# Optimization experiments

Measured on AMD Instinct MI355X. Metric: run time of the kernel, lower is better.

## Reference

```python
import jax, jax.numpy as jnp
import numpy as np

EPS = 1e-7
CP_NUM = 16
P_NUM_TOTAL = 1024
P_PER_SEG = P_NUM_TOTAL // CP_NUM  # 64, matches int(p_num / cp_num)
ALPHA = 0.5


def setup_inputs() -> dict:
    key = jax.random.key(0)
    cps = jax.random.normal(key, (16384, CP_NUM, 2), dtype=jnp.float32)
    return {"cps": cps}


def reference(cps):
    # Centripetal Catmull-Rom spline sampling (closed curve), fully vectorized
    # over segments and sample points instead of the original double Python loop.
    B, S, D = cps.shape  # S == cp_num
    P = P_PER_SEG

    # Close the curve: append first control point.  [B, S+1, D]
    cc = jnp.concatenate([cps, cps[:, :1, :]], axis=1)

    # Boundary extension lengths (detached in the original via .detach_()).
    l01 = jax.lax.stop_gradient(
        jnp.sqrt(jnp.sum((cc[:, 0] - cc[:, 1]) ** 2, axis=-1) + EPS))[:, None]
    llast = jax.lax.stop_gradient(
        jnp.sqrt(jnp.sum((cc[:, -1] - cc[:, -2]) ** 2, axis=-1) + EPS))[:, None]
    aux_first = cc[:, 0] - l01 / llast * (cc[:, -1] - cc[:, -2])
    aux_last = cc[:, -1] + llast / l01 * (cc[:, 1] - cc[:, 0])
    # Auxiliary control points. [B, S+3, D]
    aux = jnp.concatenate([aux_first[:, None], cc, aux_last[:, None]], axis=1)

    # Centripetal knot vector: t[i] = t[i-1] + ||aux_i - aux_{i-1}||^alpha (detached).
    seg_len = jnp.sqrt(jnp.sum((aux[:, 1:] - aux[:, :-1]) ** 2, axis=-1)) ** ALPHA
    t = jnp.concatenate(
        [jnp.zeros((B, 1), dtype=cps.dtype), jnp.cumsum(seg_len, axis=1)], axis=1)
    t = jax.lax.stop_gradient(t)  # [B, S+3]

    idx = jnp.arange(S)
    # Knot windows per segment, broadcast to [B, S, 1, 1].
    t0 = t[:, idx][:, :, None, None]
    t1 = t[:, idx + 1][:, :, None, None]
    t2 = t[:, idx + 2][:, :, None, None]
    t3 = t[:, idx + 3][:, :, None, None]
    # Control point windows per segment, broadcast to [B, S, 1, D].
    P0 = aux[:, idx][:, :, None, :]
    P1 = aux[:, idx + 1][:, :, None, :]
    P2 = aux[:, idx + 2][:, :, None, :]
    P3 = aux[:, idx + 3][:, :, None, :]

    # batch_linspace(t1, t2, P): P points inclusive of both endpoints. [B,S,P,1]
    u = jnp.linspace(0.0, 1.0, P, dtype=cps.dtype)[None, None, :, None]
    tv = t1 + (t2 - t1) * u

    # Barry-Goldman pyramid of weighted blends.
    x01 = (t1 - tv) / (t1 - t0) * P0 + (tv - t0) / (t1 - t0) * P1
    x12 = (t2 - tv) / (t2 - t1) * P1 + (tv - t1) / (t2 - t1) * P2
    x23 = (t3 - tv) / (t3 - t2) * P2 + (tv - t2) / (t3 - t2) * P3
    x012 = (t2 - tv) / (t2 - t0) * x01 + (tv - t0) / (t2 - t0) * x12
    x123 = (t3 - tv) / (t3 - t1) * x12 + (tv - t1) / (t3 - t1) * x23
    pts = (t2 - tv) / (t2 - t1) * x012 + (tv - t1) / (t2 - t1) * x123  # [B,S,P,D]

    return pts.reshape(B, S * P, D)
```

## Files before the change

### kernel.cpp

```cpp
#include <hip/hip_runtime.h>

#define CP_NUM 16
#define SEGS   16
#define WPB    4
#define BLK    (WPB * 64)

__global__ __launch_bounds__(BLK) void spline_poly_kernel(
    const float* __restrict__ cps, float* __restrict__ out, int nb)
{
    __shared__ __align__(16) float s_cp [WPB][CP_NUM * 2];
    __shared__ __align__(16) float s_aux[WPB][19 * 2];
    __shared__ __align__(16) float s_t  [WPB][20];
    __shared__ __align__(16) float s_seg[WPB][SEGS][12];

    const int lane = threadIdx.x & 63;
    const int wv   = threadIdx.x >> 6;
    const int b    = blockIdx.x * WPB + wv;
    if (b >= nb) return;

    if (lane < 8) {
        reinterpret_cast<float4*>(s_cp[wv])[lane] =
            reinterpret_cast<const float4*>(cps + (size_t)b * (CP_NUM * 2))[lane];
    }
    __builtin_amdgcn_wave_barrier();

    if (lane < 19) {
        const float c0x = s_cp[wv][0],  c0y = s_cp[wv][1];
        const float c1x = s_cp[wv][2],  c1y = s_cp[wv][3];
        const float cLx = s_cp[wv][30], cLy = s_cp[wv][31];
        const float dx01 = c0x - c1x, dy01 = c0y - c1y;
        const float l01   = sqrtf(dx01 * dx01 + dy01 * dy01 + 1e-7f);
        const float dxl = c0x - cLx, dyl = c0y - cLy;
        const float llast = sqrtf(dxl * dxl + dyl * dyl + 1e-7f);
        float ax, ay;
        if (lane == 0) {
            const float r = l01 / llast;
            ax = c0x - r * dxl;  ay = c0y - r * dyl;
        } else if (lane <= CP_NUM) {
            ax = s_cp[wv][(lane - 1) * 2];  ay = s_cp[wv][(lane - 1) * 2 + 1];
        } else if (lane == CP_NUM + 1) {
            ax = c0x;  ay = c0y;
        } else {
            const float r = llast / l01;
            ax = c0x + r * (c1x - c0x);  ay = c0y + r * (c1y - c0y);
        }
        s_aux[wv][lane * 2]     = ax;
        s_aux[wv][lane * 2 + 1] = ay;
    }
    __builtin_amdgcn_wave_barrier();

    float len = 0.f;
    if (lane < 18) {
        const float dx = s_aux[wv][(lane + 1) * 2]     - s_aux[wv][lane * 2];
        const float dy = s_aux[wv][(lane + 1) * 2 + 1] - s_aux[wv][lane * 2 + 1];
        len = sqrtf(sqrtf(dx * dx + dy * dy));
    }
    #pragma unroll
    for (int d = 1; d < 32; d <<= 1) {
        const float n = __shfl_up(len, d);
        if (lane >= d) len += n;
    }
    if (lane == 0) s_t[wv][0] = 0.f;
    if (lane < 18) s_t[wv][lane + 1] = len;
    __builtin_amdgcn_wave_barrier();

    if (lane < SEGS) {
        const float t0 = s_t[wv][lane];
        const float t1 = s_t[wv][lane + 1];
        const float t2 = s_t[wv][lane + 2];
        const float t3 = s_t[wv][lane + 3];
        const float A  = t1 - t0, Bk = t2 - t1, C = t3 - t2;
        const float BC = Bk + C;
        const float r10 = 1.f / A;
        const float r21 = 1.f / Bk;
        const float r32 = 1.f / C;
        const float r20 = 1.f / (A + Bk);
        const float r31 = 1.f / BC;

        float* sp = s_seg[wv][lane];
        #pragma unroll
        for (int d = 0; d < 2; ++d) {
            const float P0 = s_aux[wv][lane * 2 + d];
            const float P1 = s_aux[wv][lane * 2 + 2 + d];
            const float P2 = s_aux[wv][lane * 2 + 4 + d];
            const float P3 = s_aux[wv][lane * 2 + 6 + d];
            const float L1c0 = P1,                              L1c1 = (P1 - P0) * r10;
            const float L2c0 = P1,                              L2c1 = (P2 - P1) * r21;
            const float L3c0 = (BC * P2 - Bk * P3) * r32,       L3c1 = (P3 - P2) * r32;
            const float Q1c0 = r20 * (Bk * L1c0 + A * L2c0);
            const float Q1c1 = r20 * (Bk * L1c1 - L1c0 + A * L2c1 + L2c0);
            const float Q1c2 = r20 * (L2c1 - L1c1);
            const float Q2c0 = r31 * (BC * L2c0);
            const float Q2c1 = r31 * (BC * L2c1 - L2c0 + L3c0);
            const float Q2c2 = r31 * (L3c1 - L2c1);
            sp[d * 4 + 0] = Q1c0;
            sp[d * 4 + 1] = Q1c1 + r21 * (Q2c0 - Q1c0);
            sp[d * 4 + 2] = Q1c2 + r21 * (Q2c1 - Q1c1);
            sp[d * 4 + 3] = r21 * (Q2c2 - Q1c2);
        }
        sp[8] = Bk;
    }
    __builtin_amdgcn_wave_barrier();

    float4* outw = reinterpret_cast<float4*>(out + (size_t)b * (SEGS * 64 * 2));
    #pragma unroll
    for (int i = 0; i < 8; ++i) {
        const int f  = lane + 64 * i;
        const int sg = f >> 5;
        const int j  = (f & 31) * 2;
        const float* sp = s_seg[wv][sg];
        const float4 cx = *reinterpret_cast<const float4*>(sp);
        const float4 cy = *reinterpret_cast<const float4*>(sp + 4);
        const float dt  = sp[8];
        const float s0 = dt * (float)j       * (1.f / 63.f);
        const float s1 = dt * (float)(j + 1) * (1.f / 63.f);
        float4 o;
        o.x = ((cx.w * s0 + cx.z) * s0 + cx.y) * s0 + cx.x;
        o.y = ((cy.w * s0 + cy.z) * s0 + cy.y) * s0 + cy.x;
        o.z = ((cx.w * s1 + cx.z) * s1 + cx.y) * s1 + cx.x;
        o.w = ((cy.w * s1 + cy.z) * s1 + cy.y) * s1 + cy.x;
        outw[f] = o;
    }
}

extern "C" void kernel_launch(void* const* d_in, const int* in_sizes, int n_in,
                              void* d_out, int out_size, void* d_ws, size_t ws_size,
                              hipStream_t stream) {
    const float* cps = (const float*)d_in[0];
    float* out = (float*)d_out;
    const int B = in_sizes[0] / (CP_NUM * 2);
    const int grid = (B + WPB - 1) / WPB;
    spline_poly_kernel<<<grid, BLK, 0, stream>>>(cps, out, B);
}
```

Before: 27.74 us.

## Replace LDS staging with wave shuffles and use nontemporal output stores

Each lane now loads its control point straight into registers. Cross-lane shuffles build the auxiliary points and knot windows, replacing the three shared-memory staging arrays and their wave barriers. The per-lane sample parameters are hoisted out of the output loop, and the output is written with nontemporal stores to avoid polluting the cache. Shuffle index wraparound for out-of-range lanes only feeds lanes whose results go unused, but it does add cross-lane traffic in exchange for less LDS use.

```diff
diff --git a/kernel.cpp b/kernel.cpp
--- a/kernel.cpp
+++ b/kernel.cpp
@@ -5,12 +5,11 @@
 #define WPB    4
 #define BLK    (WPB * 64)
 
+typedef float f32x4 __attribute__((ext_vector_type(4)));
+
 __global__ __launch_bounds__(BLK) void spline_poly_kernel(
     const float* __restrict__ cps, float* __restrict__ out, int nb)
 {
-    __shared__ __align__(16) float s_cp [WPB][CP_NUM * 2];
-    __shared__ __align__(16) float s_aux[WPB][19 * 2];
-    __shared__ __align__(16) float s_t  [WPB][20];
     __shared__ __align__(16) float s_seg[WPB][SEGS][12];
 
     const int lane = threadIdx.x & 63;
@@ -18,41 +17,33 @@
     const int b    = blockIdx.x * WPB + wv;
     if (b >= nb) return;
 
-    if (lane < 8) {
-        reinterpret_cast<float4*>(s_cp[wv])[lane] =
-            reinterpret_cast<const float4*>(cps + (size_t)b * (CP_NUM * 2))[lane];
+    const float* cpb = cps + (size_t)b * (CP_NUM * 2);
+
+    const int src = (lane - 1) & 15;
+    const float2 ld = *reinterpret_cast<const float2*>(cpb + src * 2);
+    const float c0x = __shfl(ld.x, 1),  c0y = __shfl(ld.y, 1);
+    const float c1x = __shfl(ld.x, 2),  c1y = __shfl(ld.y, 2);
+    const float cLx = __shfl(ld.x, 16), cLy = __shfl(ld.y, 16);
+
+    const float dx01 = c0x - c1x, dy01 = c0y - c1y;
+    const float l01   = sqrtf(dx01 * dx01 + dy01 * dy01 + 1e-7f);
+    const float dxl = c0x - cLx, dyl = c0y - cLy;
+    const float llast = sqrtf(dxl * dxl + dyl * dyl + 1e-7f);
+
+    float ax = ld.x, ay = ld.y;
+    if (lane == 0) {
+        const float r = l01 / llast;
+        ax = c0x - r * dxl;  ay = c0y - r * dyl;
+    } else if (lane == 18) {
+        const float r = llast / l01;
+        ax = c0x + r * (c1x - c0x);  ay = c0y + r * (c1y - c0y);
     }
-    __builtin_amdgcn_wave_barrier();
 
-    if (lane < 19) {
-        const float c0x = s_cp[wv][0],  c0y = s_cp[wv][1];
-        const float c1x = s_cp[wv][2],  c1y = s_cp[wv][3];
-        const float cLx = s_cp[wv][30], cLy = s_cp[wv][31];
-        const float dx01 = c0x - c1x, dy01 = c0y - c1y;
-        const float l01   = sqrtf(dx01 * dx01 + dy01 * dy01 + 1e-7f);
-        const float dxl = c0x - cLx, dyl = c0y - cLy;
-        const float llast = sqrtf(dxl * dxl + dyl * dyl + 1e-7f);
-        float ax, ay;
-        if (lane == 0) {
-            const float r = l01 / llast;
-            ax = c0x - r * dxl;  ay = c0y - r * dyl;
-        } else if (lane <= CP_NUM) {
-            ax = s_cp[wv][(lane - 1) * 2];  ay = s_cp[wv][(lane - 1) * 2 + 1];
-        } else if (lane == CP_NUM + 1) {
-            ax = c0x;  ay = c0y;
-        } else {
-            const float r = llast / l01;
-            ax = c0x + r * (c1x - c0x);  ay = c0y + r * (c1y - c0y);
-        }
-        s_aux[wv][lane * 2]     = ax;
-        s_aux[wv][lane * 2 + 1] = ay;
-    }
-    __builtin_amdgcn_wave_barrier();
-
+    const float nax = __shfl(ax, lane + 1);
+    const float nay = __shfl(ay, lane + 1);
     float len = 0.f;
     if (lane < 18) {
-        const float dx = s_aux[wv][(lane + 1) * 2]     - s_aux[wv][lane * 2];
-        const float dy = s_aux[wv][(lane + 1) * 2 + 1] - s_aux[wv][lane * 2 + 1];
+        const float dx = nax - ax, dy = nay - ay;
         len = sqrtf(sqrtf(dx * dx + dy * dy));
     }
     #pragma unroll
@@ -60,15 +51,17 @@
         const float n = __shfl_up(len, d);
         if (lane >= d) len += n;
     }
-    if (lane == 0) s_t[wv][0] = 0.f;
-    if (lane < 18) s_t[wv][lane + 1] = len;
-    __builtin_amdgcn_wave_barrier();
+
+    const float tm1 = __shfl(len, (lane - 1) & 63);
+    const float t0  = (lane == 0) ? 0.f : tm1;
+    const float t1  = len;
+    const float t2  = __shfl(len, lane + 1);
+    const float t3  = __shfl(len, lane + 2);
+    const float p1x = nax,                  p1y = nay;
+    const float p2x = __shfl(ax, lane + 2), p2y = __shfl(ay, lane + 2);
+    const float p3x = __shfl(ax, lane + 3), p3y = __shfl(ay, lane + 3);
 
     if (lane < SEGS) {
-        const float t0 = s_t[wv][lane];
-        const float t1 = s_t[wv][lane + 1];
-        const float t2 = s_t[wv][lane + 2];
-        const float t3 = s_t[wv][lane + 3];
         const float A  = t1 - t0, Bk = t2 - t1, C = t3 - t2;
         const float BC = Bk + C;
         const float r10 = 1.f / A;
@@ -80,13 +73,13 @@
         float* sp = s_seg[wv][lane];
         #pragma unroll
         for (int d = 0; d < 2; ++d) {
-            const float P0 = s_aux[wv][lane * 2 + d];
-            const float P1 = s_aux[wv][lane * 2 + 2 + d];
-            const float P2 = s_aux[wv][lane * 2 + 4 + d];
-            const float P3 = s_aux[wv][lane * 2 + 6 + d];
-            const float L1c0 = P1,                              L1c1 = (P1 - P0) * r10;
-            const float L2c0 = P1,                              L2c1 = (P2 - P1) * r21;
-            const float L3c0 = (BC * P2 - Bk * P3) * r32,       L3c1 = (P3 - P2) * r32;
+            const float P0 = d ? ay  : ax;
+            const float P1 = d ? p1y : p1x;
+            const float P2 = d ? p2y : p2x;
+            const float P3 = d ? p3y : p3x;
+            const float L1c0 = P1,                        L1c1 = (P1 - P0) * r10;
+            const float L2c0 = P1,                        L2c1 = (P2 - P1) * r21;
+            const float L3c0 = (BC * P2 - Bk * P3) * r32, L3c1 = (P3 - P2) * r32;
             const float Q1c0 = r20 * (Bk * L1c0 + A * L2c0);
             const float Q1c1 = r20 * (Bk * L1c1 - L1c0 + A * L2c1 + L2c0);
             const float Q1c2 = r20 * (L2c1 - L1c1);
@@ -102,24 +95,24 @@
     }
     __builtin_amdgcn_wave_barrier();
 
-    float4* outw = reinterpret_cast<float4*>(out + (size_t)b * (SEGS * 64 * 2));
+    f32x4* outw = reinterpret_cast<f32x4*>(out + (size_t)b * (SEGS * 64 * 2));
+    const int   hi = lane >> 5;
+    const float q0 = (float)((lane & 31) * 2)     * (1.f / 63.f);
+    const float q1 = (float)((lane & 31) * 2 + 1) * (1.f / 63.f);
     #pragma unroll
     for (int i = 0; i < 8; ++i) {
-        const int f  = lane + 64 * i;
-        const int sg = f >> 5;
-        const int j  = (f & 31) * 2;
-        const float* sp = s_seg[wv][sg];
-        const float4 cx = *reinterpret_cast<const float4*>(sp);
-        const float4 cy = *reinterpret_cast<const float4*>(sp + 4);
-        const float dt  = sp[8];
-        const float s0 = dt * (float)j       * (1.f / 63.f);
-        const float s1 = dt * (float)(j + 1) * (1.f / 63.f);
-        float4 o;
+        const float* sp = s_seg[wv][2 * i + hi];
+        const f32x4 cx = *reinterpret_cast<const f32x4*>(sp);
+        const f32x4 cy = *reinterpret_cast<const f32x4*>(sp + 4);
+        const float dt = sp[8];
+        const float s0 = dt * q0;
+        const float s1 = dt * q1;
+        f32x4 o;
         o.x = ((cx.w * s0 + cx.z) * s0 + cx.y) * s0 + cx.x;
         o.y = ((cy.w * s0 + cy.z) * s0 + cy.y) * s0 + cy.x;
         o.z = ((cx.w * s1 + cx.z) * s1 + cx.y) * s1 + cx.x;
         o.w = ((cy.w * s1 + cy.z) * s1 + cy.y) * s1 + cy.x;
-        outw[f] = o;
+        __builtin_nontemporal_store(o, &outw[lane + 64 * i]);
     }
 }
 
```

Result: slower. 30.51 us (+10.0%).
